# Kernel tuning notes

Measured on AMD Instinct MI355X. Metric: run time of the kernel, lower is better.

Reference implementation:

```python
import jax, jax.numpy as jnp
import numpy as np
import math

N_NODES = 20000
N_EDGES = 320000
MUL = 64          # multiplicity of each irrep block
N_BASIS = 10
N_HID = 100
W_NUMEL = 4 * MUL  # 4 'uvu' instructions, v=1


def setup_inputs() -> dict:
    key = jax.random.key(0)
    ks = jax.random.split(key, 16)
    node_input = jax.random.normal(ks[0], (N_NODES, 4 * MUL), dtype=jnp.float32)  # 64x0e + 64x1o -> 64 + 192
    node_attr = jnp.ones((N_NODES, 1), dtype=jnp.float32)
    node_deg = jax.random.randint(ks[1], (N_NODES, 1), 1, 33).astype(jnp.float32)
    edge_src = jax.random.randint(ks[2], (N_EDGES,), 0, N_NODES)
    edge_dst = jax.random.randint(ks[3], (N_EDGES,), 0, N_NODES)
    edge_attr = jax.random.normal(ks[4], (N_EDGES, 4), dtype=jnp.float32)  # sh: 1x0e + 1x1o
    edge_length_embedded = jax.random.uniform(ks[5], (N_EDGES, N_BASIS), dtype=jnp.float32)
    # FullyConnectedTensorProduct weights (node_attr is 1x0e -> per-irrep linear mixing)
    W_li0 = jax.random.normal(ks[6], (MUL, MUL), dtype=jnp.float32)
    W_li1 = jax.random.normal(ks[7], (MUL, MUL), dtype=jnp.float32)
    W_lm0 = jax.random.normal(ks[8], (MUL, MUL), dtype=jnp.float32)
    W_lm1 = jax.random.normal(ks[9], (MUL, MUL), dtype=jnp.float32)
    # radial MLP: number_of_basis -> radial_neurons -> weight_numel (no bias, e3nn FullyConnectedNet style)
    W_mlp1 = jax.random.normal(ks[10], (N_BASIS, N_HID), dtype=jnp.float32)
    W_mlp2 = jax.random.normal(ks[11], (N_HID, W_NUMEL), dtype=jnp.float32)
    # linear_output: irreps_mid (128x0e + 128x1o) x 1x0e -> 64x0e + 64x1o
    W_lo0 = jax.random.normal(ks[12], (2 * MUL, MUL), dtype=jnp.float32)
    W_lo1 = jax.random.normal(ks[13], (2 * MUL, MUL), dtype=jnp.float32)
    return dict(node_input=node_input, node_attr=node_attr, node_deg=node_deg,
                edge_attr=edge_attr, edge_length_embedded=edge_length_embedded,
                W_li0=W_li0, W_li1=W_li1, W_lm0=W_lm0, W_lm1=W_lm1,
                W_mlp1=W_mlp1, W_mlp2=W_mlp2, W_lo0=W_lo0, W_lo1=W_lo1,
                edge_src=edge_src, edge_dst=edge_dst)


def _split(x):
    # split 64x0e + 64x1o feature vector into scalar [*,64] and vector [*,64,3] parts
    s = x[..., :MUL]
    v = x[..., MUL:].reshape(x.shape[:-1] + (MUL, 3))
    return s, v


def _fctp(s, v, W0, W1, attr, fan_in):
    # FullyConnectedTensorProduct with 1x0e attr: per-irrep linear, path-normalized
    inv = 1.0 / math.sqrt(fan_in)
    o0 = jnp.einsum('nu,uk->nk', s, W0) * attr * inv
    o1 = jnp.einsum('num,uk->nkm', v, W1) * attr[..., None] * inv
    return o0, o1


def reference(node_input, node_attr, node_deg, edge_attr, edge_length_embedded,
              W_li0, W_li1, W_lm0, W_lm1, W_mlp1, W_mlp2, W_lo0, W_lo1,
              edge_src, edge_dst):
    N = node_input.shape[0]
    x0, x1 = _split(node_input)

    # linear_input then degree pre-normalization
    f0, f1 = _fctp(x0, x1, W_li0, W_li1, node_attr, MUL)
    deg_isqrt = 1.0 / jnp.sqrt(node_deg)            # [N,1]
    f0 = f0 * deg_isqrt
    f1 = f1 * deg_isqrt[..., None]

    # linear_mask (skip path)
    m0, m1 = _fctp(x0, x1, W_lm0, W_lm1, node_attr, MUL)

    # radial MLP -> per-edge tensor-product weights [E, 256]
    h = jax.nn.silu(edge_length_embedded @ W_mlp1 / math.sqrt(N_BASIS))
    ew = (h @ W_mlp2) / math.sqrt(N_HID)
    wa, wb, wc, wd = ew[:, :MUL], ew[:, MUL:2*MUL], ew[:, 2*MUL:3*MUL], ew[:, 3*MUL:]

    # gather source-node features per edge
    g0 = f0[edge_src]                                # [E,64]
    g1 = f1[edge_src]                                # [E,64,3]
    y0 = edge_attr[:, 0]                             # [E]   1x0e
    y1 = edge_attr[:, 1:4]                           # [E,3] 1x1o

    # 'uvu' tensor product paths (block-diagonal equivariant contractions)
    m0a = wa * g0 * y0[:, None]                                        # 0e x 0e -> 0e
    m0b = wb * jnp.einsum('eum,em->eu', g1, y1) / math.sqrt(3.0)       # 1o x 1o -> 0e
    m1a = wc[:, :, None] * g0[:, :, None] * y1[:, None, :]             # 0e x 1o -> 1o
    m1b = wd[:, :, None] * g1 * y0[:, None, None]                      # 1o x 0e -> 1o

    # scatter-sum into destination nodes (irreps_mid = 128x0e + 128x1o)
    s_mid = jax.ops.segment_sum(jnp.concatenate([m0a, m0b], axis=1), edge_dst, num_segments=N)          # [N,128]
    v_mid = jax.ops.segment_sum(jnp.concatenate([m1a, m1b], axis=1), edge_dst, num_segments=N)          # [N,128,3]

    # degree post-normalization
    s_mid = s_mid * deg_isqrt
    v_mid = v_mid * deg_isqrt[..., None]

    # linear_output
    o0, o1 = _fctp(s_mid, v_mid, W_lo0, W_lo1, node_attr, 2 * MUL)

    # masked skip combination; output_mask is all ones here (every out irrep is reachable)
    c_s, c_x = math.sin(math.pi / 8), math.cos(math.pi / 8)
    out0 = c_s * m0 + c_x * o0                       # [N,64]
    out1 = c_s * m1 + c_x * o1                       # [N,64,3]
    return jnp.concatenate([out0, out1.reshape(N, 3 * MUL)], axis=1)  # [N,256]
```

## Files before the change

kernel.cpp:

```cpp
#include <hip/hip_runtime.h>
#include <hip/hip_bf16.h>
#include <math.h>

#define N_NODES 20000
#define N_EDGES 320000

#define INV1   0.31622776601683794f
#define SC2    0.1f
#define IS3    0.5773502691896258f
#define C_S    0.3826834323650898f
#define C_X    0.9238795325112867f
#define INV64  0.125f
#define INVLO  0.08838834764831845f

typedef short     short8 __attribute__((ext_vector_type(8)));
typedef float     f32x4  __attribute__((ext_vector_type(4)));

__device__ __forceinline__ float silu_f(float x) {
    float e = __builtin_amdgcn_exp2f(-1.44269504088896f * x);
    return x * __builtin_amdgcn_rcpf(1.0f + e);
}
__device__ __forceinline__ unsigned short f2bf(float x) {
    __hip_bfloat16 h = __float2bfloat16(x);
    return *reinterpret_cast<unsigned short*>(&h);
}
__device__ __forceinline__ float bf2f(unsigned short u) {
    __hip_bfloat16 h;
    *reinterpret_cast<unsigned short*>(&h) = u;
    return __bfloat162float(h);
}

__global__ __launch_bounds__(256) void k_node_in(
    const float* __restrict__ ni, const float* __restrict__ attr,
    const float* __restrict__ deg,
    const float* __restrict__ Wli0, const float* __restrict__ Wli1,
    const float* __restrict__ Wlm0, const float* __restrict__ Wlm1,
    ushort4* __restrict__ fvb, float* __restrict__ out)
{
    __shared__ float raw[4][256];
    const int wave = threadIdx.x >> 6;
    const int lane = threadIdx.x & 63;
    const int n = blockIdx.x * 4 + wave;

    const float* row = ni + (size_t)n * 256;
    raw[wave][lane      ] = row[lane      ];
    raw[wave][lane + 64 ] = row[lane + 64 ];
    raw[wave][lane + 128] = row[lane + 128];
    raw[wave][lane + 192] = row[lane + 192];
    __syncthreads();

    float f0 = 0.f, m0 = 0.f;
    float f1x = 0.f, f1y = 0.f, f1z = 0.f;
    float m1x = 0.f, m1y = 0.f, m1z = 0.f;
    #pragma unroll 4
    for (int t = 0; t < 64; ++t) {
        float xs  = raw[wave][t];
        float xv0 = raw[wave][64 + t*3    ];
        float xv1 = raw[wave][64 + t*3 + 1];
        float xv2 = raw[wave][64 + t*3 + 2];
        float a0 = Wli0[t*64 + lane];
        float a1 = Wli1[t*64 + lane];
        float b0 = Wlm0[t*64 + lane];
        float b1 = Wlm1[t*64 + lane];
        f0  += xs  * a0;   m0  += xs  * b0;
        f1x += xv0 * a1;   f1y += xv1 * a1;   f1z += xv2 * a1;
        m1x += xv0 * b1;   m1y += xv1 * b1;   m1z += xv2 * b1;
    }

    const float a   = attr[n] * INV64;
    const float dis = 1.0f / sqrtf(deg[n]);
    const float fa  = a * dis;

    ushort4 pk;
    pk.x = f2bf(f0  * fa);
    pk.y = f2bf(f1x * fa);
    pk.z = f2bf(f1y * fa);
    pk.w = f2bf(f1z * fa);
    fvb[(size_t)n * 64 + lane] = pk;

    float* orow = out + (size_t)n * 256;
    orow[lane] = C_S * m0 * a;
    orow[64 + lane*3    ] = C_S * m1x * a;
    orow[64 + lane*3 + 1] = C_S * m1y * a;
    orow[64 + lane*3 + 2] = C_S * m1z * a;
}

__global__ __launch_bounds__(256) void k_prep(
    const int* __restrict__ edst, int* __restrict__ hist,
    const float* __restrict__ W2, const float* __restrict__ W1,
    unsigned short* __restrict__ w2t, unsigned short* __restrict__ w1t)
{
    const int b = blockIdx.x;
    if (b < N_EDGES / 256) {
        const int e = b * 256 + threadIdx.x;
        atomicAdd(&hist[edst[e]], 1);
    } else {
        const int i = (b - N_EDGES / 256) * 256 + threadIdx.x;
        if (i < 32768) {
            const int n = i >> 7, k = i & 127;
            w2t[i] = (k < 100) ? f2bf(W2[k*256 + n] * SC2) : (unsigned short)0;
        } else if (i < 32768 + 3584) {
            const int j = i - 32768;
            const int n = j >> 5, k = j & 31;
            w1t[j] = (k < 10 && n < 100) ? f2bf(W1[k*100 + n] * INV1)
                                         : (unsigned short)0;
        }
    }
}

__global__ __launch_bounds__(1024) void k_scan(const int* __restrict__ hist,
                                               int* __restrict__ starts,
                                               int* __restrict__ cursor) {
    __shared__ int part[1024];
    const int t = threadIdx.x;
    const int C = 20;
    const int base = t * C;
    int s = 0;
    for (int i = 0; i < C; ++i) {
        const int idx = base + i;
        if (idx < N_NODES) s += hist[idx];
    }
    part[t] = s;
    __syncthreads();
    for (int off = 1; off < 1024; off <<= 1) {
        int v = (t >= off) ? part[t - off] : 0;
        __syncthreads();
        part[t] += v;
        __syncthreads();
    }
    int run = part[t] - s;
    for (int i = 0; i < C; ++i) {
        const int idx = base + i;
        if (idx < N_NODES) {
            starts[idx] = run;
            cursor[idx] = run;
            run += hist[idx];
        }
    }
    if (t == 1023) starts[N_NODES] = N_EDGES;
}

__global__ __launch_bounds__(256) void k_scatter(
    const int* __restrict__ esrc, const int* __restrict__ edst,
    const float4* __restrict__ eattr4, const float* __restrict__ elen,
    int* __restrict__ cursor, int* __restrict__ esrc_s,
    float4* __restrict__ eattrs, unsigned short* __restrict__ elen_sb)
{
    const int e = blockIdx.x * 256 + threadIdx.x;
    if (e < N_EDGES) {
        const int p = atomicAdd(&cursor[edst[e]], 1);
        esrc_s[p] = esrc[e];
        eattrs[p] = eattr4[e];
        const float* el = elen + (size_t)e * 10;
        unsigned short v[32];
        #pragma unroll
        for (int b = 0; b < 10; ++b) v[b] = f2bf(el[b]);
        #pragma unroll
        for (int b = 10; b < 32; ++b) v[b] = 0;
        short8* dst = (short8*)(elen_sb + (size_t)p * 32);
        #pragma unroll
        for (int s = 0; s < 4; ++s) {
            short8 pk;
            #pragma unroll
            for (int j = 0; j < 8; ++j) pk[j] = (short)v[s*8 + j];
            dst[s] = pk;
        }
    }
}

__global__ __launch_bounds__(256, 4) void k_mlp(
    const unsigned short* __restrict__ elen_sb,
    const unsigned short* __restrict__ w1t,
    const unsigned short* __restrict__ w2t,
    unsigned int* __restrict__ ew2u)
{
    __shared__ unsigned short Hs[128 * 136];
    const int t    = threadIdx.x;
    const int w    = t >> 6;
    const int lane = t & 63;
    const int m15  = lane & 15;
    const int q    = lane >> 4;
    const int eb   = w * 32;
    const int e0   = blockIdx.x * 128;

    short8 xa0 = *(const short8*)(elen_sb + (size_t)(e0 + eb      + m15)*32 + q*8);
    short8 xa1 = *(const short8*)(elen_sb + (size_t)(e0 + eb + 16 + m15)*32 + q*8);

    short8 bw[7];
    #pragma unroll
    for (int nt = 0; nt < 7; ++nt)
        bw[nt] = *(const short8*)(w1t + (nt*16 + m15)*32 + q*8);

    {
        const int r = eb + (lane >> 1);
        const int c = 112 + (lane & 1) * 8;
        short8 z = {0,0,0,0,0,0,0,0};
        *(short8*)&Hs[r*136 + c] = z;
    }

    #pragma unroll
    for (int nt = 0; nt < 7; ++nt) {
        f32x4 z4 = {0.f, 0.f, 0.f, 0.f};
        f32x4 h0 = __builtin_amdgcn_mfma_f32_16x16x32_bf16(bw[nt], xa0, z4, 0, 0, 0);
        f32x4 h1 = __builtin_amdgcn_mfma_f32_16x16x32_bf16(bw[nt], xa1, z4, 0, 0, 0);
        uint2 d0, d1;
        d0.x = (unsigned int)f2bf(silu_f(h0[0])) | ((unsigned int)f2bf(silu_f(h0[1])) << 16);
        d0.y = (unsigned int)f2bf(silu_f(h0[2])) | ((unsigned int)f2bf(silu_f(h0[3])) << 16);
        d1.x = (unsigned int)f2bf(silu_f(h1[0])) | ((unsigned int)f2bf(silu_f(h1[1])) << 16);
        d1.y = (unsigned int)f2bf(silu_f(h1[2])) | ((unsigned int)f2bf(silu_f(h1[3])) << 16);
        *(uint2*)&Hs[(eb      + m15)*136 + nt*16 + q*4] = d0;
        *(uint2*)&Hs[(eb + 16 + m15)*136 + nt*16 + q*4] = d1;
    }

    short8 A0[4], A1[4];
    #pragma unroll
    for (int s = 0; s < 4; ++s) {
        A0[s] = *(const short8*)&Hs[(eb      + m15)*136 + s*32 + q*8];
        A1[s] = *(const short8*)&Hs[(eb + 16 + m15)*136 + s*32 + q*8];
    }

    #pragma unroll
    for (int nt4 = 0; nt4 < 4; ++nt4) {
        f32x4 acc[4][2];
        #pragma unroll
        for (int g = 0; g < 4; ++g) {
            acc[g][0] = (f32x4){0.f,0.f,0.f,0.f};
            acc[g][1] = (f32x4){0.f,0.f,0.f,0.f};
        }
        #pragma unroll
        for (int s = 0; s < 4; ++s) {
            #pragma unroll
            for (int g = 0; g < 4; ++g) {
                short8 B = *(const short8*)(w2t
                          + ((size_t)((nt4 + g*4)*16 + m15) << 7) + s*32 + q*8);
                acc[g][0] = __builtin_amdgcn_mfma_f32_16x16x32_bf16(B, A0[s], acc[g][0], 0, 0, 0);
                acc[g][1] = __builtin_amdgcn_mfma_f32_16x16x32_bf16(B, A1[s], acc[g][1], 0, 0, 0);
            }
        }
        #pragma unroll
        for (int h = 0; h < 2; ++h) {
            const int E = e0 + eb + h*16 + m15;
            unsigned int* p = ew2u + (size_t)E*128 + (nt4*16 + q*4)*2;
            uint4 U0, U1;
            U0.x = (unsigned int)f2bf(acc[0][h][0]) | ((unsigned int)f2bf(acc[1][h][0]) << 16);
            U0.y = (unsigned int)f2bf(acc[2][h][0]) | ((unsigned int)f2bf(acc[3][h][0]) << 16);
            U0.z = (unsigned int)f2bf(acc[0][h][1]) | ((unsigned int)f2bf(acc[1][h][1]) << 16);
            U0.w = (unsigned int)f2bf(acc[2][h][1]) | ((unsigned int)f2bf(acc[3][h][1]) << 16);
            U1.x = (unsigned int)f2bf(acc[0][h][2]) | ((unsigned int)f2bf(acc[1][h][2]) << 16);
            U1.y = (unsigned int)f2bf(acc[2][h][2]) | ((unsigned int)f2bf(acc[3][h][2]) << 16);
            U1.z = (unsigned int)f2bf(acc[0][h][3]) | ((unsigned int)f2bf(acc[1][h][3]) << 16);
            U1.w = (unsigned int)f2bf(acc[2][h][3]) | ((unsigned int)f2bf(acc[3][h][3]) << 16);
            *(uint4*)(p)     = U0;
            *(uint4*)(p + 4) = U1;
        }
    }
}

__global__ __launch_bounds__(256) void k_gather(
    const int* __restrict__ starts, const int* __restrict__ esrc_s,
    const float4* __restrict__ eattrs,
    const uint2* __restrict__ ew2,
    const ushort4* __restrict__ fvb,
    const float* __restrict__ attr, const float* __restrict__ deg,
    const float* __restrict__ Wlo0, const float* __restrict__ Wlo1,
    float* __restrict__ out)
{
    __shared__ float sm[4][512];
    const int wave = threadIdx.x >> 6;
    const int lane = threadIdx.x & 63;
    const int n = blockIdx.x * 4 + wave;

    const int beg = starts[n], end = starts[n + 1];
    float sA=0.f, sB=0.f;
    float vA0=0.f, vA1=0.f, vA2=0.f;
    float vB0=0.f, vB1=0.f, vB2=0.f;

    for (int base = beg; base < end; base += 64) {
        const int cnt = min(64, end - base);
        int    srcv = 0;
        float4 eav  = make_float4(0.f, 0.f, 0.f, 0.f);
        if (lane < cnt) {
            srcv = esrc_s[base + lane];
            eav  = eattrs[base + lane];
        }
        #pragma unroll 2
        for (int j = 0; j < cnt; ++j) {
            const int   src = __shfl(srcv, j);
            const float y0  = __shfl(eav.x, j);
            const float y10 = __shfl(eav.y, j);
            const float y11 = __shfl(eav.z, j);
            const float y12 = __shfl(eav.w, j);

            const uint2 u2 = ew2[(size_t)(base + j)*64 + lane];
            const float wa = bf2f((unsigned short)(u2.x & 0xFFFFu));
            const float wb = bf2f((unsigned short)(u2.x >> 16));
            const float wc = bf2f((unsigned short)(u2.y & 0xFFFFu));
            const float wd = bf2f((unsigned short)(u2.y >> 16));

            const ushort4 g4 = fvb[(size_t)src * 64 + lane];
            const float g0  = bf2f(g4.x);
            const float g10 = bf2f(g4.y);
            const float g11 = bf2f(g4.z);
            const float g12 = bf2f(g4.w);

            const float dotv = g10*y10 + g11*y11 + g12*y12;
            sA += wa * g0 * y0;
            sB += wb * dotv;
            const float t0 = wc * g0;
            vA0 += t0 * y10;  vA1 += t0 * y11;  vA2 += t0 * y12;
            const float t1 = wd * y0;
            vB0 += t1 * g10;  vB1 += t1 * g11;  vB2 += t1 * g12;
        }
    }

    const float dis = 1.0f / sqrtf(deg[n]);
    sm[wave][lane            ] = sA * dis;
    sm[wave][64  + lane      ] = sB * IS3 * dis;
    sm[wave][128 + lane      ] = vA0 * dis;
    sm[wave][128 + 64 + lane ] = vB0 * dis;
    sm[wave][256 + lane      ] = vA1 * dis;
    sm[wave][256 + 64 + lane ] = vB1 * dis;
    sm[wave][384 + lane      ] = vA2 * dis;
    sm[wave][384 + 64 + lane ] = vB2 * dis;
    __syncthreads();

    float o0=0.f, o1x=0.f, o1y=0.f, o1z=0.f;
    #pragma unroll 4
    for (int c = 0; c < 128; ++c) {
        const float w0 = Wlo0[c*64 + lane];
        const float w1 = Wlo1[c*64 + lane];
        o0  += sm[wave][c]         * w0;
        o1x += sm[wave][128 + c]   * w1;
        o1y += sm[wave][256 + c]   * w1;
        o1z += sm[wave][384 + c]   * w1;
    }

    const float a = attr[n] * INVLO;
    float* orow = out + (size_t)n * 256;
    orow[lane] += C_X * o0 * a;
    orow[64 + lane*3    ] += C_X * o1x * a;
    orow[64 + lane*3 + 1] += C_X * o1y * a;
    orow[64 + lane*3 + 2] += C_X * o1z * a;
}

__global__ __launch_bounds__(256) void k_node_in_legacy(
    const float* __restrict__ ni, const float* __restrict__ attr,
    const float* __restrict__ deg,
    const float* __restrict__ Wli0, const float* __restrict__ Wli1,
    const float* __restrict__ Wlm0, const float* __restrict__ Wlm1,
    float* __restrict__ f, float* __restrict__ out)
{
    __shared__ float raw[4][256];
    const int wave = threadIdx.x >> 6;
    const int lane = threadIdx.x & 63;
    const int n = blockIdx.x * 4 + wave;

    const float* row = ni + (size_t)n * 256;
    raw[wave][lane      ] = row[lane      ];
    raw[wave][lane + 64 ] = row[lane + 64 ];
    raw[wave][lane + 128] = row[lane + 128];
    raw[wave][lane + 192] = row[lane + 192];
    __syncthreads();

    float f0 = 0.f, m0 = 0.f;
    float f1x = 0.f, f1y = 0.f, f1z = 0.f;
    float m1x = 0.f, m1y = 0.f, m1z = 0.f;
    for (int t = 0; t < 64; ++t) {
        float xs  = raw[wave][t];
        float xv0 = raw[wave][64 + t*3    ];
        float xv1 = raw[wave][64 + t*3 + 1];
        float xv2 = raw[wave][64 + t*3 + 2];
        float a0 = Wli0[t*64 + lane];
        float a1 = Wli1[t*64 + lane];
        float b0 = Wlm0[t*64 + lane];
        float b1 = Wlm1[t*64 + lane];
        f0  += xs  * a0;   m0  += xs  * b0;
        f1x += xv0 * a1;   f1y += xv1 * a1;   f1z += xv2 * a1;
        m1x += xv0 * b1;   m1y += xv1 * b1;   m1z += xv2 * b1;
    }

    const float a   = attr[n] * INV64;
    const float dis = 1.0f / sqrtf(deg[n]);
    const float fa  = a * dis;

    float* fr = f + (size_t)n * 256;
    fr[lane      ] = f0  * fa;
    fr[64  + lane] = f1x * fa;
    fr[128 + lane] = f1y * fa;
    fr[192 + lane] = f1z * fa;

    float* orow = out + (size_t)n * 256;
    orow[lane] = C_S * m0 * a;
    orow[64 + lane*3    ] = C_S * m1x * a;
    orow[64 + lane*3 + 1] = C_S * m1y * a;
    orow[64 + lane*3 + 2] = C_S * m1z * a;
}

__global__ __launch_bounds__(256) void k_edge_legacy(
    const float* __restrict__ eattr, const float* __restrict__ elen,
    const float* __restrict__ W1, const float* __restrict__ W2,
    const int* __restrict__ esrc, const int* __restrict__ edst,
    const float* __restrict__ f, float* __restrict__ acc)
{
    __shared__ float hsh[4][104];
    const int wave = threadIdx.x >> 6;
    const int lane = threadIdx.x & 63;
    const int e = blockIdx.x * 4 + wave;

    const float* el = elen + (size_t)e * 10;
    float elr[10];
    #pragma unroll
    for (int b = 0; b < 10; ++b) elr[b] = el[b];

    float a1 = 0.f;
    #pragma unroll
    for (int b = 0; b < 10; ++b) a1 += elr[b] * W1[b*100 + lane];
    hsh[wave][lane] = silu_f(a1 * INV1);
    if (lane < 36) {
        float a2 = 0.f;
        #pragma unroll
        for (int b = 0; b < 10; ++b) a2 += elr[b] * W1[b*100 + 64 + lane];
        hsh[wave][64 + lane] = silu_f(a2 * INV1);
    }
    __syncthreads();

    float wa = 0.f, wb = 0.f, wc = 0.f, wd = 0.f;
    for (int j = 0; j < 100; ++j) {
        float hj = hsh[wave][j];
        const float* wr = W2 + j*256;
        wa += hj * wr[lane      ];
        wb += hj * wr[64  + lane];
        wc += hj * wr[128 + lane];
        wd += hj * wr[192 + lane];
    }
    wa *= SC2; wb *= SC2; wc *= SC2; wd *= SC2;

    const int src = esrc[e];
    const int dst = edst[e];
    const float y0  = eattr[e*4 + 0];
    const float y10 = eattr[e*4 + 1];
    const float y11 = eattr[e*4 + 2];
    const float y12 = eattr[e*4 + 3];

    const float* fr = f + (size_t)src * 256;
    const float g0  = fr[lane      ];
    const float g10 = fr[64  + lane];
    const float g11 = fr[128 + lane];
    const float g12 = fr[192 + lane];

    const float dotv = g10*y10 + g11*y11 + g12*y12;

    float* ar = acc + (size_t)dst * 512;
    atomicAdd(ar + lane,                  wa * g0 * y0);
    atomicAdd(ar + 64 + lane,             wb * dotv * IS3);
    atomicAdd(ar + 128 +   0 + lane,      wc * g0 * y10);
    atomicAdd(ar + 128 + 128 + lane,      wc * g0 * y11);
    atomicAdd(ar + 128 + 256 + lane,      wc * g0 * y12);
    atomicAdd(ar + 128 +   0 + 64 + lane, wd * g10 * y0);
    atomicAdd(ar + 128 + 128 + 64 + lane, wd * g11 * y0);
    atomicAdd(ar + 128 + 256 + 64 + lane, wd * g12 * y0);
}

__global__ __launch_bounds__(256) void k_node_out_legacy(
    const float* __restrict__ acc, const float* __restrict__ attr,
    const float* __restrict__ deg, const float* __restrict__ Wlo0,
    const float* __restrict__ Wlo1, float* __restrict__ out)
{
    __shared__ float sm[4][512];
    const int wave = threadIdx.x >> 6;
    const int lane = threadIdx.x & 63;
    const int n = blockIdx.x * 4 + wave;

    const float dis = 1.0f / sqrtf(deg[n]);
    const float* ar = acc + (size_t)n * 512;
    for (int i = lane; i < 512; i += 64) sm[wave][i] = ar[i] * dis;
    __syncthreads();

    float o0 = 0.f, o1x = 0.f, o1y = 0.f, o1z = 0.f;
    for (int c = 0; c < 128; ++c) {
        float w0 = Wlo0[c*64 + lane];
        float w1 = Wlo1[c*64 + lane];
        o0  += sm[wave][c]        * w0;
        o1x += sm[wave][128 + c]  * w1;
        o1y += sm[wave][256 + c]  * w1;
        o1z += sm[wave][384 + c]  * w1;
    }

    const float a = attr[n] * INVLO;
    float* orow = out + (size_t)n * 256;
    orow[lane] += C_X * o0 * a;
    orow[64 + lane*3    ] += C_X * o1x * a;
    orow[64 + lane*3 + 1] += C_X * o1y * a;
    orow[64 + lane*3 + 2] += C_X * o1z * a;
}

extern "C" void kernel_launch(void* const* d_in, const int* in_sizes, int n_in,
                              void* d_out, int out_size, void* d_ws, size_t ws_size,
                              hipStream_t stream) {
    const float* ni    = (const float*)d_in[0];
    const float* attr  = (const float*)d_in[1];
    const float* deg   = (const float*)d_in[2];
    const float* eattr = (const float*)d_in[3];
    const float* elen  = (const float*)d_in[4];
    const float* Wli0  = (const float*)d_in[5];
    const float* Wli1  = (const float*)d_in[6];
    const float* Wlm0  = (const float*)d_in[7];
    const float* Wlm1  = (const float*)d_in[8];
    const float* Wm1   = (const float*)d_in[9];
    const float* Wm2   = (const float*)d_in[10];
    const float* Wlo0  = (const float*)d_in[11];
    const float* Wlo1  = (const float*)d_in[12];
    const int*   esrc  = (const int*)d_in[13];
    const int*   edst  = (const int*)d_in[14];

    float* out = (float*)d_out;

    char* wsb = (char*)d_ws;
    size_t off = 0;
    ushort4* fvb = (ushort4*)(wsb + off);               off += (size_t)N_NODES * 64 * 8;
    uint2* ew2 = (uint2*)(wsb + off);                   off += (size_t)N_EDGES * 64 * 8;
    unsigned short* elen_sb = (unsigned short*)(wsb + off); off += (size_t)N_EDGES * 32 * 2;
    float4* eattrs = (float4*)(wsb + off);              off += (size_t)N_EDGES * 16;
    int* esrc_s = (int*)(wsb + off);                    off += (size_t)N_EDGES * 4;
    unsigned short* w2t = (unsigned short*)(wsb + off); off += 32768 * 2;
    unsigned short* w1t = (unsigned short*)(wsb + off); off += 3584 * 2;
    int* starts = (int*)(wsb + off);                    off += (size_t)(N_NODES + 4) * 4;
    int* hist   = (int*)(wsb + off);                    off += (size_t)N_NODES * 4;
    int* cursor = (int*)(wsb + off);                    off += (size_t)N_NODES * 4;
    const size_t need_fast = off;

    if (ws_size >= need_fast) {
        hipMemsetAsync(hist, 0, (size_t)N_NODES * sizeof(int), stream);
        k_node_in<<<N_NODES / 4, 256, 0, stream>>>(ni, attr, deg, Wli0, Wli1,
                                                   Wlm0, Wlm1, fvb, out);
        k_prep   <<<N_EDGES / 256 + 144, 256, 0, stream>>>(edst, hist,
                                                           Wm2, Wm1, w2t, w1t);
        k_scan   <<<1, 1024, 0, stream>>>(hist, starts, cursor);
        k_scatter<<<N_EDGES / 256, 256, 0, stream>>>(esrc, edst,
                                                     (const float4*)eattr, elen,
                                                     cursor, esrc_s, eattrs, elen_sb);
        k_mlp    <<<N_EDGES / 128, 256, 0, stream>>>(elen_sb, w1t, w2t,
                                                     (unsigned int*)ew2);
        k_gather <<<N_NODES / 4, 256, 0, stream>>>(starts, esrc_s, eattrs,
                                                   ew2, fvb, attr, deg,
                                                   Wlo0, Wlo1, out);
    } else {
        float* f   = (float*)d_ws;
        float* acc = f + (size_t)N_NODES * 256;
        hipMemsetAsync(acc, 0, (size_t)N_NODES * 512 * sizeof(float), stream);
        k_node_in_legacy<<<N_NODES / 4, 256, 0, stream>>>(ni, attr, deg, Wli0, Wli1,
                                                          Wlm0, Wlm1, f, out);
        k_edge_legacy<<<N_EDGES / 4, 256, 0, stream>>>(eattr, elen, Wm1, Wm2,
                                                       esrc, edst, f, acc);
        k_node_out_legacy<<<N_NODES / 4, 256, 0, stream>>>(acc, attr, deg,
                                                           Wlo0, Wlo1, out);
    }
}
```

Baseline: 408.6 us.

## Fuse radial MLP into per-node gather to drop edge-weight buffer

Removes the separate k_mlp kernel and computes each edge's radial MLP weights inside the gather kernel, 16 edges at a time per wave, using MFMA and keeping the results in LDS. This removes the write and read-back of the bf16 per-edge weight buffer (roughly 160 MB of traffic) and one kernel launch. In exchange, MFMA work is done in chunks of 16 that are often only partly filled, since average degree is about 16 and varies between nodes. w2t is reloaded per chunk, and LDS use per block goes up. The output linear layer now broadcasts values with shuffles instead of going through shared memory, which also drops a __syncthreads.

```diff
diff --git a/kernel.cpp b/kernel.cpp
--- a/kernel.cpp
+++ b/kernel.cpp
@@ -13,8 +13,9 @@
 #define INV64  0.125f
 #define INVLO  0.08838834764831845f
 
-typedef short     short8 __attribute__((ext_vector_type(8)));
-typedef float     f32x4  __attribute__((ext_vector_type(4)));
+typedef short     short8  __attribute__((ext_vector_type(8)));
+typedef short     short4v __attribute__((ext_vector_type(4)));
+typedef float     f32x4   __attribute__((ext_vector_type(4)));
 
 __device__ __forceinline__ float silu_f(float x) {
     float e = __builtin_amdgcn_exp2f(-1.44269504088896f * x);
@@ -168,23 +169,25 @@
     }
 }
 
-__global__ __launch_bounds__(256, 4) void k_mlp(
+__global__ __launch_bounds__(256) void k_gather(
+    const int* __restrict__ starts, const int* __restrict__ esrc_s,
+    const float4* __restrict__ eattrs,
     const unsigned short* __restrict__ elen_sb,
     const unsigned short* __restrict__ w1t,
     const unsigned short* __restrict__ w2t,
-    unsigned int* __restrict__ ew2u)
-{
-    __shared__ unsigned short Hs[128 * 136];
-    const int t    = threadIdx.x;
-    const int w    = t >> 6;
-    const int lane = t & 63;
+    const ushort4* __restrict__ fvb,
+    const float* __restrict__ attr, const float* __restrict__ deg,
+    const float* __restrict__ Wlo0, const float* __restrict__ Wlo1,
+    float* __restrict__ out)
+{
+    __shared__ unsigned short Hs[4][16 * 136];
+    __shared__ uint2 ewl[4][16 * 64];
+
+    const int wave = threadIdx.x >> 6;
+    const int lane = threadIdx.x & 63;
     const int m15  = lane & 15;
     const int q    = lane >> 4;
-    const int eb   = w * 32;
-    const int e0   = blockIdx.x * 128;
-
-    short8 xa0 = *(const short8*)(elen_sb + (size_t)(e0 + eb      + m15)*32 + q*8);
-    short8 xa1 = *(const short8*)(elen_sb + (size_t)(e0 + eb + 16 + m15)*32 + q*8);
+    const int n    = blockIdx.x * 4 + wave;
 
     short8 bw[7];
     #pragma unroll
@@ -192,98 +195,73 @@
         bw[nt] = *(const short8*)(w1t + (nt*16 + m15)*32 + q*8);
 
     {
-        const int r = eb + (lane >> 1);
-        const int c = 112 + (lane & 1) * 8;
-        short8 z = {0,0,0,0,0,0,0,0};
-        *(short8*)&Hs[r*136 + c] = z;
-    }
-
-    #pragma unroll
-    for (int nt = 0; nt < 7; ++nt) {
-        f32x4 z4 = {0.f, 0.f, 0.f, 0.f};
-        f32x4 h0 = __builtin_amdgcn_mfma_f32_16x16x32_bf16(bw[nt], xa0, z4, 0, 0, 0);
-        f32x4 h1 = __builtin_amdgcn_mfma_f32_16x16x32_bf16(bw[nt], xa1, z4, 0, 0, 0);
-        uint2 d0, d1;
-        d0.x = (unsigned int)f2bf(silu_f(h0[0])) | ((unsigned int)f2bf(silu_f(h0[1])) << 16);
-        d0.y = (unsigned int)f2bf(silu_f(h0[2])) | ((unsigned int)f2bf(silu_f(h0[3])) << 16);
-        d1.x = (unsigned int)f2bf(silu_f(h1[0])) | ((unsigned int)f2bf(silu_f(h1[1])) << 16);
-        d1.y = (unsigned int)f2bf(silu_f(h1[2])) | ((unsigned int)f2bf(silu_f(h1[3])) << 16);
-        *(uint2*)&Hs[(eb      + m15)*136 + nt*16 + q*4] = d0;
-        *(uint2*)&Hs[(eb + 16 + m15)*136 + nt*16 + q*4] = d1;
-    }
-
-    short8 A0[4], A1[4];
-    #pragma unroll
-    for (int s = 0; s < 4; ++s) {
-        A0[s] = *(const short8*)&Hs[(eb      + m15)*136 + s*32 + q*8];
-        A1[s] = *(const short8*)&Hs[(eb + 16 + m15)*136 + s*32 + q*8];
-    }
-
-    #pragma unroll
-    for (int nt4 = 0; nt4 < 4; ++nt4) {
-        f32x4 acc[4][2];
-        #pragma unroll
-        for (int g = 0; g < 4; ++g) {
-            acc[g][0] = (f32x4){0.f,0.f,0.f,0.f};
-            acc[g][1] = (f32x4){0.f,0.f,0.f,0.f};
-        }
-        #pragma unroll
-        for (int s = 0; s < 4; ++s) {
-            #pragma unroll
-            for (int g = 0; g < 4; ++g) {
-                short8 B = *(const short8*)(w2t
-                          + ((size_t)((nt4 + g*4)*16 + m15) << 7) + s*32 + q*8);
-                acc[g][0] = __builtin_amdgcn_mfma_f32_16x16x32_bf16(B, A0[s], acc[g][0], 0, 0, 0);
-                acc[g][1] = __builtin_amdgcn_mfma_f32_16x16x32_bf16(B, A1[s], acc[g][1], 0, 0, 0);
-            }
-        }
-        #pragma unroll
-        for (int h = 0; h < 2; ++h) {
-            const int E = e0 + eb + h*16 + m15;
-            unsigned int* p = ew2u + (size_t)E*128 + (nt4*16 + q*4)*2;
-            uint4 U0, U1;
-            U0.x = (unsigned int)f2bf(acc[0][h][0]) | ((unsigned int)f2bf(acc[1][h][0]) << 16);
-            U0.y = (unsigned int)f2bf(acc[2][h][0]) | ((unsigned int)f2bf(acc[3][h][0]) << 16);
-            U0.z = (unsigned int)f2bf(acc[0][h][1]) | ((unsigned int)f2bf(acc[1][h][1]) << 16);
-            U0.w = (unsigned int)f2bf(acc[2][h][1]) | ((unsigned int)f2bf(acc[3][h][1]) << 16);
-            U1.x = (unsigned int)f2bf(acc[0][h][2]) | ((unsigned int)f2bf(acc[1][h][2]) << 16);
-            U1.y = (unsigned int)f2bf(acc[2][h][2]) | ((unsigned int)f2bf(acc[3][h][2]) << 16);
-            U1.z = (unsigned int)f2bf(acc[0][h][3]) | ((unsigned int)f2bf(acc[1][h][3]) << 16);
-            U1.w = (unsigned int)f2bf(acc[2][h][3]) | ((unsigned int)f2bf(acc[3][h][3]) << 16);
-            *(uint4*)(p)     = U0;
-            *(uint4*)(p + 4) = U1;
-        }
-    }
-}
-
-__global__ __launch_bounds__(256) void k_gather(
-    const int* __restrict__ starts, const int* __restrict__ esrc_s,
-    const float4* __restrict__ eattrs,
-    const uint2* __restrict__ ew2,
-    const ushort4* __restrict__ fvb,
-    const float* __restrict__ attr, const float* __restrict__ deg,
-    const float* __restrict__ Wlo0, const float* __restrict__ Wlo1,
-    float* __restrict__ out)
-{
-    __shared__ float sm[4][512];
-    const int wave = threadIdx.x >> 6;
-    const int lane = threadIdx.x & 63;
-    const int n = blockIdx.x * 4 + wave;
+        short4v z = {0,0,0,0};
+        *(short4v*)&Hs[wave][(lane >> 2)*136 + 112 + (lane & 3)*4] = z;
+    }
 
     const int beg = starts[n], end = starts[n + 1];
     float sA=0.f, sB=0.f;
     float vA0=0.f, vA1=0.f, vA2=0.f;
     float vB0=0.f, vB1=0.f, vB2=0.f;
 
-    for (int base = beg; base < end; base += 64) {
-        const int cnt = min(64, end - base);
+    for (int base = beg; base < end; base += 16) {
+        const int cnt = min(16, end - base);
+
         int    srcv = 0;
         float4 eav  = make_float4(0.f, 0.f, 0.f, 0.f);
         if (lane < cnt) {
             srcv = esrc_s[base + lane];
             eav  = eattrs[base + lane];
         }
-        #pragma unroll 2
+
+        short8 xa = {0,0,0,0,0,0,0,0};
+        if (m15 < cnt)
+            xa = *(const short8*)(elen_sb + (size_t)(base + m15)*32 + q*8);
+
+        #pragma unroll
+        for (int nt = 0; nt < 7; ++nt) {
+            f32x4 z4 = {0.f, 0.f, 0.f, 0.f};
+            f32x4 h = __builtin_amdgcn_mfma_f32_16x16x32_bf16(bw[nt], xa, z4, 0, 0, 0);
+            uint2 d;
+            d.x = (unsigned int)f2bf(silu_f(h[0])) | ((unsigned int)f2bf(silu_f(h[1])) << 16);
+            d.y = (unsigned int)f2bf(silu_f(h[2])) | ((unsigned int)f2bf(silu_f(h[3])) << 16);
+            *(uint2*)&Hs[wave][m15*136 + nt*16 + q*4] = d;
+        }
+
+        short8 A[4];
+        #pragma unroll
+        for (int s = 0; s < 4; ++s)
+            A[s] = *(const short8*)&Hs[wave][m15*136 + s*32 + q*8];
+
+        #pragma unroll
+        for (int nt4 = 0; nt4 < 4; ++nt4) {
+            f32x4 ag0 = {0.f,0.f,0.f,0.f}, ag1 = {0.f,0.f,0.f,0.f};
+            f32x4 ag2 = {0.f,0.f,0.f,0.f}, ag3 = {0.f,0.f,0.f,0.f};
+            #pragma unroll
+            for (int s = 0; s < 4; ++s) {
+                short8 B0 = *(const short8*)(w2t + ((size_t)((nt4     )*16 + m15) << 7) + s*32 + q*8);
+                short8 B1 = *(const short8*)(w2t + ((size_t)((nt4 +  4)*16 + m15) << 7) + s*32 + q*8);
+                short8 B2 = *(const short8*)(w2t + ((size_t)((nt4 +  8)*16 + m15) << 7) + s*32 + q*8);
+                short8 B3 = *(const short8*)(w2t + ((size_t)((nt4 + 12)*16 + m15) << 7) + s*32 + q*8);
+                ag0 = __builtin_amdgcn_mfma_f32_16x16x32_bf16(B0, A[s], ag0, 0, 0, 0);
+                ag1 = __builtin_amdgcn_mfma_f32_16x16x32_bf16(B1, A[s], ag1, 0, 0, 0);
+                ag2 = __builtin_amdgcn_mfma_f32_16x16x32_bf16(B2, A[s], ag2, 0, 0, 0);
+                ag3 = __builtin_amdgcn_mfma_f32_16x16x32_bf16(B3, A[s], ag3, 0, 0, 0);
+            }
+            uint4 U0, U1;
+            U0.x = (unsigned int)f2bf(ag0[0]) | ((unsigned int)f2bf(ag1[0]) << 16);
+            U0.y = (unsigned int)f2bf(ag2[0]) | ((unsigned int)f2bf(ag3[0]) << 16);
+            U0.z = (unsigned int)f2bf(ag0[1]) | ((unsigned int)f2bf(ag1[1]) << 16);
+            U0.w = (unsigned int)f2bf(ag2[1]) | ((unsigned int)f2bf(ag3[1]) << 16);
+            U1.x = (unsigned int)f2bf(ag0[2]) | ((unsigned int)f2bf(ag1[2]) << 16);
+            U1.y = (unsigned int)f2bf(ag2[2]) | ((unsigned int)f2bf(ag3[2]) << 16);
+            U1.z = (unsigned int)f2bf(ag0[3]) | ((unsigned int)f2bf(ag1[3]) << 16);
+            U1.w = (unsigned int)f2bf(ag2[3]) | ((unsigned int)f2bf(ag3[3]) << 16);
+            uint2* p = &ewl[wave][m15*64 + nt4*16 + q*4];
+            *(uint4*)(p)     = U0;
+            *(uint4*)(p + 2) = U1;
+        }
+
         for (int j = 0; j < cnt; ++j) {
             const int   src = __shfl(srcv, j);
             const float y0  = __shfl(eav.x, j);
@@ -291,7 +269,7 @@
             const float y11 = __shfl(eav.z, j);
             const float y12 = __shfl(eav.w, j);
 
-            const uint2 u2 = ew2[(size_t)(base + j)*64 + lane];
+            const uint2 u2 = ewl[wave][j*64 + lane];
             const float wa = bf2f((unsigned short)(u2.x & 0xFFFFu));
             const float wb = bf2f((unsigned short)(u2.x >> 16));
             const float wc = bf2f((unsigned short)(u2.y & 0xFFFFu));
@@ -314,25 +292,22 @@
     }
 
     const float dis = 1.0f / sqrtf(deg[n]);
-    sm[wave][lane            ] = sA * dis;
-    sm[wave][64  + lane      ] = sB * IS3 * dis;
-    sm[wave][128 + lane      ] = vA0 * dis;
-    sm[wave][128 + 64 + lane ] = vB0 * dis;
-    sm[wave][256 + lane      ] = vA1 * dis;
-    sm[wave][256 + 64 + lane ] = vB1 * dis;
-    sm[wave][384 + lane      ] = vA2 * dis;
-    sm[wave][384 + 64 + lane ] = vB2 * dis;
-    __syncthreads();
+    const float s0v = sA * dis;
+    const float s1v = sB * IS3 * dis;
+    const float va0 = vA0 * dis, va1 = vA1 * dis, va2 = vA2 * dis;
+    const float vb0 = vB0 * dis, vb1 = vB1 * dis, vb2 = vB2 * dis;
 
     float o0=0.f, o1x=0.f, o1y=0.f, o1z=0.f;
     #pragma unroll 4
-    for (int c = 0; c < 128; ++c) {
-        const float w0 = Wlo0[c*64 + lane];
-        const float w1 = Wlo1[c*64 + lane];
-        o0  += sm[wave][c]         * w0;
-        o1x += sm[wave][128 + c]   * w1;
-        o1y += sm[wave][256 + c]   * w1;
-        o1z += sm[wave][384 + c]   * w1;
+    for (int c = 0; c < 64; ++c) {
+        const float w0a = Wlo0[c*64 + lane];
+        const float w0b = Wlo0[(64 + c)*64 + lane];
+        const float w1a = Wlo1[c*64 + lane];
+        const float w1b = Wlo1[(64 + c)*64 + lane];
+        o0  += __shfl(s0v, c)*w0a + __shfl(s1v, c)*w0b;
+        o1x += __shfl(va0, c)*w1a + __shfl(vb0, c)*w1b;
+        o1y += __shfl(va1, c)*w1a + __shfl(vb1, c)*w1b;
+        o1z += __shfl(va2, c)*w1a + __shfl(vb2, c)*w1b;
     }
 
     const float a = attr[n] * INVLO;
@@ -518,7 +493,6 @@
     char* wsb = (char*)d_ws;
     size_t off = 0;
     ushort4* fvb = (ushort4*)(wsb + off);               off += (size_t)N_NODES * 64 * 8;
-    uint2* ew2 = (uint2*)(wsb + off);                   off += (size_t)N_EDGES * 64 * 8;
     unsigned short* elen_sb = (unsigned short*)(wsb + off); off += (size_t)N_EDGES * 32 * 2;
     float4* eattrs = (float4*)(wsb + off);              off += (size_t)N_EDGES * 16;
     int* esrc_s = (int*)(wsb + off);                    off += (size_t)N_EDGES * 4;
@@ -539,10 +513,9 @@
         k_scatter<<<N_EDGES / 256, 256, 0, stream>>>(esrc, edst,
                                                      (const float4*)eattr, elen,
                                                      cursor, esrc_s, eattrs, elen_sb);
-        k_mlp    <<<N_EDGES / 128, 256, 0, stream>>>(elen_sb, w1t, w2t,
-                                                     (unsigned int*)ew2);
         k_gather <<<N_NODES / 4, 256, 0, stream>>>(starts, esrc_s, eattrs,
-                                                   ew2, fvb, attr, deg,
+                                                   elen_sb, w1t, w2t,
+                                                   fvb, attr, deg,
                                                    Wlo0, Wlo1, out);
     } else {
         float* f   = (float*)d_ws;
```

Result: slower. 700.1 us (+71.3%).
